# Performance work log

Hardware: AMD Instinct MI355X
Metric: run time of the kernel (lower is better)

Reference implementation:

```python
import jax, jax.numpy as jnp
import numpy as np

B, N, D_U = 32, 4096, 64
D = 128          # mlp_dim == model dim after MLP
H = 2            # n_heads
DH = D // H


def setup_inputs() -> dict:
    key = jax.random.key(0)
    ks = jax.random.split(key, 16)
    sc = lambda fan_in: 1.0 / np.sqrt(fan_in)
    inp = {
        "u": jax.random.normal(ks[0], (B, N, D_U), dtype=jnp.float32),
        "x": jax.random.uniform(ks[1], (B, N, 2), dtype=jnp.float32),
        # MLP params: [D_U -> D -> D], gelu after each hidden layer
        "W1": jax.random.normal(ks[2], (D_U, D), dtype=jnp.float32) * sc(D_U),
        "b1": jnp.zeros((D,), jnp.float32),
        "W2": jax.random.normal(ks[3], (D, D), dtype=jnp.float32) * sc(D),
        "b2": jnp.zeros((D,), jnp.float32),
        # learned pooling query (nn.Embed(1, D))
        "embed": jax.random.normal(ks[4], (1, D), dtype=jnp.float32),
        # multihead linear attention projections
        "Wq": jax.random.normal(ks[5], (D, D), dtype=jnp.float32) * sc(D),
        "bq": jnp.zeros((D,), jnp.float32),
        "Wk": jax.random.normal(ks[6], (D, D), dtype=jnp.float32) * sc(D),
        "bk": jnp.zeros((D,), jnp.float32),
        "Wv": jax.random.normal(ks[7], (D, D), dtype=jnp.float32) * sc(D),
        "bv": jnp.zeros((D,), jnp.float32),
        "Wo": jax.random.normal(ks[8], (D, D), dtype=jnp.float32) * sc(D),
        "bo": jnp.zeros((D,), jnp.float32),
    }
    return inp


def reference(u, x, W1, b1, W2, b2, embed, Wq, bq, Wk, bk, Wv, bv, Wo, bo):
    # MLP on set elements: [B, N, D_U] -> [B, N, D]
    z = jax.nn.gelu(u @ W1 + b1)
    z = jax.nn.gelu(z @ W2 + b2)

    n = z.shape[1]
    # learned query broadcast over batch: [B, 1, D]
    s = jnp.broadcast_to(embed[None, :, :], (z.shape[0], 1, z.shape[-1]))

    # multihead linear (Galerkin-style, softmax-free) attention
    q = (s @ Wq + bq).reshape(z.shape[0], 1, H, DH)   # [B, 1, H, DH]
    k = (z @ Wk + bk).reshape(z.shape[0], n, H, DH)   # [B, N, H, DH]
    v = (z @ Wv + bv).reshape(z.shape[0], n, H, DH)   # [B, N, H, DH]

    # context = K^T V / N per head: [B, H, DH, DH]
    context = jnp.einsum("bnhd,bnhe->bhde", k, v) / n
    out = jnp.einsum("bqhd,bhde->bqhe", q, context)   # [B, 1, H, DH]
    out = out.reshape(z.shape[0], 1, D) @ Wo + bo     # [B, 1, D]

    return out[:, 0, :]                               # [B, D]
```

## Files before the change

### kernel.cpp

```cpp
#include <hip/hip_runtime.h>
#include <math.h>

#define Bsz 32
#define Nn  4096
#define DU  64
#define Dm  128

#define GRID_MLP 256
#define BPB 8

#define WS_WKQ 0
#define WS_BKQ 256
#define WS_CNT 288
#define WS_A   320
#define WS_S   384
#define WS_WP  8576

#define H1STR 136

typedef short frag_ab __attribute__((ext_vector_type(8)));
typedef float frag_cd __attribute__((ext_vector_type(4)));

__device__ __forceinline__ unsigned short f2bf(float x) {
    union { float f; unsigned int u; } c; c.f = x;
    unsigned int r = c.u + 0x7fffu + ((c.u >> 16) & 1u);
    return (unsigned short)(r >> 16);
}

__device__ __forceinline__ float gelu_fast(float x) {
    float t = x * x;
    float a = x * fmaf(t, -0.1029432f, -2.3022081f);
    float e = __builtin_amdgcn_exp2f(a);
    return x * __builtin_amdgcn_rcpf(1.0f + e);
}

__global__ __launch_bounds__(256) void precompute_kernel(
    const float* __restrict__ embed, const float* __restrict__ Wq,
    const float* __restrict__ bq, const float* __restrict__ Wk,
    const float* __restrict__ bk, const float* __restrict__ W1,
    const float* __restrict__ W2, float* __restrict__ ws)
{
    __shared__ float qv[128];
    const int tid = threadIdx.x;
    const int bid = blockIdx.x;

    if (bid < 12) {
        const int e = bid * 256 + tid;
        const int f = e >> 6, L = e & 63;
        const int quad = L >> 4, n = L & 15;
        const float* src;
        int ks, nt;
        if (f < 16) { src = W1; ks = f >> 3;        nt = f & 7; }
        else        { src = W2; ks = (f - 16) >> 3; nt = (f - 16) & 7; }
        const int kb = ks * 32 + quad * 8;
        const int c  = nt * 16 + n;
        unsigned int p[4];
        #pragma unroll
        for (int jj = 0; jj < 4; ++jj) {
            unsigned int lo = f2bf(src[(kb + 2 * jj)     * Dm + c]);
            unsigned int hi = f2bf(src[(kb + 2 * jj + 1) * Dm + c]);
            p[jj] = lo | (hi << 16);
        }
        ((uint4*)(ws + WS_WP))[e] = make_uint4(p[0], p[1], p[2], p[3]);
    } else {
        if (tid < 128) {
            float s = bq[tid];
            #pragma unroll 8
            for (int j = 0; j < 128; ++j) s += embed[j] * Wq[j * 128 + tid];
            qv[tid] = s;
        }
        __syncthreads();
        if (tid < 128) {
            float s0 = 0.f, s1 = 0.f;
            #pragma unroll 8
            for (int dh = 0; dh < 64; ++dh) {
                s0 += Wk[tid * 128 + dh]      * qv[dh];
                s1 += Wk[tid * 128 + 64 + dh] * qv[64 + dh];
            }
            ws[WS_WKQ + tid]       = s0;
            ws[WS_WKQ + 128 + tid] = s1;
        }
        if (tid < 2) {
            float s = 0.f;
            for (int dh = 0; dh < 64; ++dh) s += bk[tid * 64 + dh] * qv[tid * 64 + dh];
            ws[WS_BKQ + tid] = s;
        }
    }
}

__global__ __launch_bounds__(1024) void mlp_pool_kernel(
    const float* __restrict__ u,  const float* __restrict__ b1,
    const float* __restrict__ b2, const float* __restrict__ Wv,
    const float* __restrict__ bv, const float* __restrict__ Wo,
    const float* __restrict__ bo, float* __restrict__ ws,
    float* __restrict__ out)
{
    __shared__ short  lds_w[48 * 512];
    __shared__ short  lds_h1[8 * 16 * H1STR];
    __shared__ float2 a2buf[8 * 16 * 2];
    __shared__ int    do_epi;

    const int tid  = threadIdx.x;
    const int wave = tid >> 6;
    const int lane = tid & 63;
    const int quad = lane >> 4;
    const int n15  = lane & 15;
    const int p    = wave >> 1;
    const int hf   = wave & 1;

    {
        const float4* src = (const float4*)(ws + WS_WP);
        float4* dst = (float4*)lds_w;
        dst[tid]        = src[tid];
        dst[tid + 1024] = src[tid + 1024];
        dst[tid + 2048] = src[tid + 2048];
    }

    float b1c[4], b2c[4], wkq0[4], wkq1[4];
    #pragma unroll
    for (int nt = 0; nt < 4; ++nt) {
        const int c = hf * 64 + nt * 16 + n15;
        b1c[nt]  = b1[c];
        b2c[nt]  = b2[c];
        wkq0[nt] = ws[WS_WKQ + c];
        wkq1[nt] = ws[WS_WKQ + 128 + c];
    }
    const float bkq0 = ws[WS_BKQ];
    const float bkq1 = ws[WS_BKQ + 1];
    __syncthreads();

    const int bb = blockIdx.x >> 3;
    const int jb = blockIdx.x & 7;
    short* h1t = lds_h1 + p * 16 * H1STR;

    float s0p[4], s1p[4];
    #pragma unroll
    for (int nt = 0; nt < 4; ++nt) { s0p[nt] = 0.f; s1p[nt] = 0.f; }
    float aA0 = 0.f, aA1 = 0.f;

    #pragma unroll 1
    for (int it = 0; it < 4; ++it) {
        const float* up = u + ((size_t)(bb * Nn + jb * 512 + it * 128 + p * 16 + n15)) * DU + quad * 8;
        float4 f0 = *(const float4*)(up);
        float4 f1 = *(const float4*)(up + 4);
        float4 f2 = *(const float4*)(up + 32);
        float4 f3 = *(const float4*)(up + 36);

        frag_ab a0, a1;
        a0[0] = (short)f2bf(f0.x); a0[1] = (short)f2bf(f0.y);
        a0[2] = (short)f2bf(f0.z); a0[3] = (short)f2bf(f0.w);
        a0[4] = (short)f2bf(f1.x); a0[5] = (short)f2bf(f1.y);
        a0[6] = (short)f2bf(f1.z); a0[7] = (short)f2bf(f1.w);
        a1[0] = (short)f2bf(f2.x); a1[1] = (short)f2bf(f2.y);
        a1[2] = (short)f2bf(f2.z); a1[3] = (short)f2bf(f2.w);
        a1[4] = (short)f2bf(f3.x); a1[5] = (short)f2bf(f3.y);
        a1[6] = (short)f2bf(f3.z); a1[7] = (short)f2bf(f3.w);

        frag_cd acc[4];
        #pragma unroll
        for (int nt = 0; nt < 4; ++nt) acc[nt] = (frag_cd){0.f, 0.f, 0.f, 0.f};
        #pragma unroll
        for (int nt = 0; nt < 4; ++nt) {
            const int f = hf * 4 + nt;
            frag_ab w0 = *(const frag_ab*)&lds_w[(f)     * 512 + lane * 8];
            acc[nt] = __builtin_amdgcn_mfma_f32_16x16x32_bf16(a0, w0, acc[nt], 0, 0, 0);
            frag_ab w1 = *(const frag_ab*)&lds_w[(8 + f) * 512 + lane * 8];
            acc[nt] = __builtin_amdgcn_mfma_f32_16x16x32_bf16(a1, w1, acc[nt], 0, 0, 0);
        }

        #pragma unroll
        for (int nt = 0; nt < 4; ++nt) {
            #pragma unroll
            for (int r = 0; r < 4; ++r) {
                float g = gelu_fast(acc[nt][r] + b1c[nt]);
                h1t[(quad * 4 + r) * H1STR + hf * 64 + nt * 16 + n15] = (short)f2bf(g);
            }
        }
        __syncthreads();

        frag_cd acc2[4];
        #pragma unroll
        for (int nt = 0; nt < 4; ++nt) acc2[nt] = (frag_cd){0.f, 0.f, 0.f, 0.f};
        #pragma unroll
        for (int ks = 0; ks < 4; ++ks) {
            frag_ab a2 = *(const frag_ab*)&h1t[n15 * H1STR + ks * 32 + quad * 8];
            #pragma unroll
            for (int nt = 0; nt < 4; ++nt) {
                frag_ab w2f = *(const frag_ab*)&lds_w[(16 + ks * 8 + hf * 4 + nt) * 512 + lane * 8];
                acc2[nt] = __builtin_amdgcn_mfma_f32_16x16x32_bf16(a2, w2f, acc2[nt], 0, 0, 0);
            }
        }

        #pragma unroll
        for (int nt = 0; nt < 4; ++nt) {
            #pragma unroll
            for (int r = 0; r < 4; ++r)
                acc2[nt][r] = gelu_fast(acc2[nt][r] + b2c[nt]);
        }

        float p0[4], p1[4];
        #pragma unroll
        for (int r = 0; r < 4; ++r) { p0[r] = 0.f; p1[r] = 0.f; }
        #pragma unroll
        for (int nt = 0; nt < 4; ++nt) {
            #pragma unroll
            for (int r = 0; r < 4; ++r) {
                p0[r] += acc2[nt][r] * wkq0[nt];
                p1[r] += acc2[nt][r] * wkq1[nt];
            }
        }
        #pragma unroll
        for (int r = 0; r < 4; ++r) {
            #pragma unroll
            for (int d = 1; d < 16; d <<= 1) {
                p0[r] += __shfl_xor(p0[r], d);
                p1[r] += __shfl_xor(p1[r], d);
            }
        }
        if (n15 == 0) {
            float* ab = (float*)a2buf;
            #pragma unroll
            for (int r = 0; r < 4; ++r) {
                const int row = quad * 4 + r;
                ab[(p * 32 + row * 2 + 0) * 2 + hf] = p0[r];
                ab[(p * 32 + row * 2 + 1) * 2 + hf] = p1[r];
            }
        }
        __syncthreads();

        #pragma unroll
        for (int r = 0; r < 4; ++r) {
            const int row = quad * 4 + r;
            float2 v0 = a2buf[p * 32 + row * 2 + 0];
            float2 v1 = a2buf[p * 32 + row * 2 + 1];
            const float al0 = v0.x + v0.y + bkq0;
            const float al1 = v1.x + v1.y + bkq1;
            #pragma unroll
            for (int nt = 0; nt < 4; ++nt) {
                s0p[nt] += al0 * acc2[nt][r];
                s1p[nt] += al1 * acc2[nt][r];
            }
            aA0 += al0; aA1 += al1;
        }
    }

    #pragma unroll
    for (int nt = 0; nt < 4; ++nt) {
        s0p[nt] += __shfl_xor(s0p[nt], 16); s0p[nt] += __shfl_xor(s0p[nt], 32);
        s1p[nt] += __shfl_xor(s1p[nt], 16); s1p[nt] += __shfl_xor(s1p[nt], 32);
    }
    aA0 += __shfl_xor(aA0, 16); aA0 += __shfl_xor(aA0, 32);
    aA1 += __shfl_xor(aA1, 16); aA1 += __shfl_xor(aA1, 32);

    if (quad == 0) {
        #pragma unroll
        for (int nt = 0; nt < 4; ++nt) {
            const int c = hf * 64 + nt * 16 + n15;
            atomicAdd(&ws[WS_S + (bb * 2 + 0) * 128 + c], s0p[nt]);
            atomicAdd(&ws[WS_S + (bb * 2 + 1) * 128 + c], s1p[nt]);
        }
    }
    if (hf == 0 && lane == 0) {
        atomicAdd(&ws[WS_A + bb * 2 + 0], aA0);
        atomicAdd(&ws[WS_A + bb * 2 + 1], aA1);
    }

    __syncthreads();
    if (tid == 0) {
        __threadfence();
        int old = atomicAdd((int*)ws + WS_CNT + bb, 1);
        do_epi = (old == BPB - 1) ? 1 : 0;
    }
    __syncthreads();

    if (do_epi) {
        float* eb     = (float*)lds_h1;
        float* e_sS   = eb;
        float* e_sA   = eb + 256;
        float* e_pool = eb + 264;
        float* e_part = eb + 392;

        if (tid < 256) e_sS[tid] = atomicAdd(&ws[WS_S + bb * 256 + tid], 0.f);
        if (tid < 2)   e_sA[tid] = atomicAdd(&ws[WS_A + bb * 2 + tid], 0.f);
        __syncthreads();

        const int i = tid & 127, seg = tid >> 7;
        const int h = i >> 6;
        if (tid < 512) {
            float dot = 0.f;
            #pragma unroll 8
            for (int d0 = 0; d0 < 32; ++d0) {
                const int d = seg * 32 + d0;
                dot += e_sS[h * 128 + d] * Wv[d * 128 + i];
            }
            e_part[tid] = dot;
        }
        __syncthreads();
        if (tid < 128)
            e_pool[i] = (e_part[i] + e_part[128 + i] + e_part[256 + i] + e_part[384 + i]
                         + e_sA[h] * bv[i]) * (1.0f / 4096.0f);
        __syncthreads();

        if (tid < 512) {
            float o = 0.f;
            #pragma unroll 8
            for (int d0 = 0; d0 < 32; ++d0) {
                const int d = seg * 32 + d0;
                o += e_pool[d] * Wo[d * 128 + i];
            }
            e_part[tid] = o;
        }
        __syncthreads();
        if (tid < 128)
            out[bb * 128 + i] = bo[i] + e_part[i] + e_part[128 + i] + e_part[256 + i] + e_part[384 + i];
    }
}

extern "C" void kernel_launch(void* const* d_in, const int* in_sizes, int n_in,
                              void* d_out, int out_size, void* d_ws, size_t ws_size,
                              hipStream_t stream) {
    const float* u     = (const float*)d_in[0];
    const float* W1    = (const float*)d_in[2];
    const float* b1    = (const float*)d_in[3];
    const float* W2    = (const float*)d_in[4];
    const float* b2    = (const float*)d_in[5];
    const float* embed = (const float*)d_in[6];
    const float* Wq    = (const float*)d_in[7];
    const float* bq    = (const float*)d_in[8];
    const float* Wk    = (const float*)d_in[9];
    const float* bk    = (const float*)d_in[10];
    const float* Wv    = (const float*)d_in[11];
    const float* bv    = (const float*)d_in[12];
    const float* Wo    = (const float*)d_in[13];
    const float* bo    = (const float*)d_in[14];
    float* ws  = (float*)d_ws;
    float* out = (float*)d_out;

    hipMemsetAsync((char*)d_ws + WS_CNT * 4, 0, (WS_WP - WS_CNT) * 4, stream);
    hipLaunchKernelGGL(precompute_kernel, dim3(13), dim3(256), 0, stream,
                       embed, Wq, bq, Wk, bk, W1, W2, ws);
    hipLaunchKernelGGL(mlp_pool_kernel, dim3(GRID_MLP), dim3(1024), 0, stream,
                       u, b1, b2, Wv, bv, Wo, bo, ws, out);
}
```

Baseline: 156.2 us.

## Fuse precompute into main kernel, prefetch u and double-buffer pooling stage

Removes the separate precompute kernel. Each block now packs W1/W2 into bf16 MFMA layout directly in LDS and computes Wk·q locally, which saves a launch and a global round trip. The main loop prefetches the next u tile into registers and double-buffers h1 and the alpha buffers. The alpha-weighted accumulation is deferred by one iteration so one __syncthreads per iteration can be dropped. In exchange, every one of the 256 blocks redundantly repacks the weights and computes the q projection. It also uses more LDS and registers.

```diff
diff --git a/kernel.cpp b/kernel.cpp
--- a/kernel.cpp
+++ b/kernel.cpp
@@ -9,12 +9,10 @@
 #define GRID_MLP 256
 #define BPB 8
 
-#define WS_WKQ 0
-#define WS_BKQ 256
 #define WS_CNT 288
 #define WS_A   320
 #define WS_S   384
-#define WS_WP  8576
+#define WS_END 8576
 
 #define H1STR 136
 
@@ -34,71 +32,21 @@
     return x * __builtin_amdgcn_rcpf(1.0f + e);
 }
 
-__global__ __launch_bounds__(256) void precompute_kernel(
-    const float* __restrict__ embed, const float* __restrict__ Wq,
-    const float* __restrict__ bq, const float* __restrict__ Wk,
-    const float* __restrict__ bk, const float* __restrict__ W1,
-    const float* __restrict__ W2, float* __restrict__ ws)
+__global__ __launch_bounds__(1024) void fused_mlp_pool_kernel(
+    const float* __restrict__ u,   const float* __restrict__ W1,
+    const float* __restrict__ b1,  const float* __restrict__ W2,
+    const float* __restrict__ b2,  const float* __restrict__ embed,
+    const float* __restrict__ Wq,  const float* __restrict__ bq,
+    const float* __restrict__ Wk,  const float* __restrict__ bk,
+    const float* __restrict__ Wv,  const float* __restrict__ bv,
+    const float* __restrict__ Wo,  const float* __restrict__ bo,
+    float* __restrict__ ws, float* __restrict__ out)
 {
-    __shared__ float qv[128];
-    const int tid = threadIdx.x;
-    const int bid = blockIdx.x;
-
-    if (bid < 12) {
-        const int e = bid * 256 + tid;
-        const int f = e >> 6, L = e & 63;
-        const int quad = L >> 4, n = L & 15;
-        const float* src;
-        int ks, nt;
-        if (f < 16) { src = W1; ks = f >> 3;        nt = f & 7; }
-        else        { src = W2; ks = (f - 16) >> 3; nt = (f - 16) & 7; }
-        const int kb = ks * 32 + quad * 8;
-        const int c  = nt * 16 + n;
-        unsigned int p[4];
-        #pragma unroll
-        for (int jj = 0; jj < 4; ++jj) {
-            unsigned int lo = f2bf(src[(kb + 2 * jj)     * Dm + c]);
-            unsigned int hi = f2bf(src[(kb + 2 * jj + 1) * Dm + c]);
-            p[jj] = lo | (hi << 16);
-        }
-        ((uint4*)(ws + WS_WP))[e] = make_uint4(p[0], p[1], p[2], p[3]);
-    } else {
-        if (tid < 128) {
-            float s = bq[tid];
-            #pragma unroll 8
-            for (int j = 0; j < 128; ++j) s += embed[j] * Wq[j * 128 + tid];
-            qv[tid] = s;
-        }
-        __syncthreads();
-        if (tid < 128) {
-            float s0 = 0.f, s1 = 0.f;
-            #pragma unroll 8
-            for (int dh = 0; dh < 64; ++dh) {
-                s0 += Wk[tid * 128 + dh]      * qv[dh];
-                s1 += Wk[tid * 128 + 64 + dh] * qv[64 + dh];
-            }
-            ws[WS_WKQ + tid]       = s0;
-            ws[WS_WKQ + 128 + tid] = s1;
-        }
-        if (tid < 2) {
-            float s = 0.f;
-            for (int dh = 0; dh < 64; ++dh) s += bk[tid * 64 + dh] * qv[tid * 64 + dh];
-            ws[WS_BKQ + tid] = s;
-        }
-    }
-}
-
-__global__ __launch_bounds__(1024) void mlp_pool_kernel(
-    const float* __restrict__ u,  const float* __restrict__ b1,
-    const float* __restrict__ b2, const float* __restrict__ Wv,
-    const float* __restrict__ bv, const float* __restrict__ Wo,
-    const float* __restrict__ bo, float* __restrict__ ws,
-    float* __restrict__ out)
-{
-    __shared__ short  lds_w[48 * 512];
-    __shared__ short  lds_h1[8 * 16 * H1STR];
-    __shared__ float2 a2buf[8 * 16 * 2];
-    __shared__ int    do_epi;
+    __shared__ short lds_w[48 * 512];
+    __shared__ short lds_h1[2][8 * 16 * H1STR];
+    __shared__ float a2buf[2][8][16][2][2];
+    __shared__ float lds_c[258];
+    __shared__ int   do_epi;
 
     const int tid  = threadIdx.x;
     const int wave = tid >> 6;
@@ -108,13 +56,49 @@
     const int p    = wave >> 1;
     const int hf   = wave & 1;
 
-    {
-        const float4* src = (const float4*)(ws + WS_WP);
-        float4* dst = (float4*)lds_w;
-        dst[tid]        = src[tid];
-        dst[tid + 1024] = src[tid + 1024];
-        dst[tid + 2048] = src[tid + 2048];
-    }
+    float* qtmp = (float*)a2buf;
+    if (tid < 128) {
+        float s = bq[tid];
+        #pragma unroll 8
+        for (int j = 0; j < 128; ++j) s += embed[j] * Wq[j * 128 + tid];
+        qtmp[tid] = s;
+    } else {
+        for (int e = tid - 128; e < 3072; e += 896) {
+            const int f = e >> 6, L = e & 63;
+            const int q2 = L >> 4, n = L & 15;
+            const float* src;
+            int ks, nt;
+            if (f < 16) { src = W1; ks = f >> 3;        nt = f & 7; }
+            else        { src = W2; ks = (f - 16) >> 3; nt = (f - 16) & 7; }
+            const int kb = ks * 32 + q2 * 8;
+            const int c  = nt * 16 + n;
+            unsigned int pk[4];
+            #pragma unroll
+            for (int jj = 0; jj < 4; ++jj) {
+                unsigned int lo = f2bf(src[(kb + 2 * jj)     * Dm + c]);
+                unsigned int hi = f2bf(src[(kb + 2 * jj + 1) * Dm + c]);
+                pk[jj] = lo | (hi << 16);
+            }
+            ((uint4*)lds_w)[e] = make_uint4(pk[0], pk[1], pk[2], pk[3]);
+        }
+    }
+    __syncthreads();
+    if (tid < 128) {
+        float s0 = 0.f, s1 = 0.f;
+        #pragma unroll 8
+        for (int dh = 0; dh < 64; ++dh) {
+            s0 += Wk[tid * 128 + dh]      * qtmp[dh];
+            s1 += Wk[tid * 128 + 64 + dh] * qtmp[64 + dh];
+        }
+        lds_c[tid]       = s0;
+        lds_c[128 + tid] = s1;
+    }
+    if (tid < 2) {
+        float s = 0.f;
+        for (int dh = 0; dh < 64; ++dh) s += bk[tid * 64 + dh] * qtmp[tid * 64 + dh];
+        lds_c[256 + tid] = s;
+    }
+    __syncthreads();
 
     float b1c[4], b2c[4], wkq0[4], wkq1[4];
     #pragma unroll
@@ -122,30 +106,30 @@
         const int c = hf * 64 + nt * 16 + n15;
         b1c[nt]  = b1[c];
         b2c[nt]  = b2[c];
-        wkq0[nt] = ws[WS_WKQ + c];
-        wkq1[nt] = ws[WS_WKQ + 128 + c];
-    }
-    const float bkq0 = ws[WS_BKQ];
-    const float bkq1 = ws[WS_BKQ + 1];
-    __syncthreads();
+        wkq0[nt] = lds_c[c];
+        wkq1[nt] = lds_c[128 + c];
+    }
+    const float bkq0 = lds_c[256];
+    const float bkq1 = lds_c[257];
 
     const int bb = blockIdx.x >> 3;
     const int jb = blockIdx.x & 7;
-    short* h1t = lds_h1 + p * 16 * H1STR;
 
     float s0p[4], s1p[4];
     #pragma unroll
     for (int nt = 0; nt < 4; ++nt) { s0p[nt] = 0.f; s1p[nt] = 0.f; }
     float aA0 = 0.f, aA1 = 0.f;
+    frag_cd zprev[4];
+    int cur = 0;
+
+    const float* ub = u + ((size_t)(bb * Nn + jb * 512 + p * 16 + n15)) * DU + quad * 8;
+    float4 f0 = *(const float4*)(ub);
+    float4 f1 = *(const float4*)(ub + 4);
+    float4 f2 = *(const float4*)(ub + 32);
+    float4 f3 = *(const float4*)(ub + 36);
 
     #pragma unroll 1
     for (int it = 0; it < 4; ++it) {
-        const float* up = u + ((size_t)(bb * Nn + jb * 512 + it * 128 + p * 16 + n15)) * DU + quad * 8;
-        float4 f0 = *(const float4*)(up);
-        float4 f1 = *(const float4*)(up + 4);
-        float4 f2 = *(const float4*)(up + 32);
-        float4 f3 = *(const float4*)(up + 36);
-
         frag_ab a0, a1;
         a0[0] = (short)f2bf(f0.x); a0[1] = (short)f2bf(f0.y);
         a0[2] = (short)f2bf(f0.z); a0[3] = (short)f2bf(f0.w);
@@ -156,6 +140,14 @@
         a1[4] = (short)f2bf(f3.x); a1[5] = (short)f2bf(f3.y);
         a1[6] = (short)f2bf(f3.z); a1[7] = (short)f2bf(f3.w);
 
+        if (it < 3) {
+            const float* un = ub + (size_t)((it + 1) * 128) * DU;
+            f0 = *(const float4*)(un);
+            f1 = *(const float4*)(un + 4);
+            f2 = *(const float4*)(un + 32);
+            f3 = *(const float4*)(un + 36);
+        }
+
         frag_cd acc[4];
         #pragma unroll
         for (int nt = 0; nt < 4; ++nt) acc[nt] = (frag_cd){0.f, 0.f, 0.f, 0.f};
@@ -168,6 +160,7 @@
             acc[nt] = __builtin_amdgcn_mfma_f32_16x16x32_bf16(a1, w1, acc[nt], 0, 0, 0);
         }
 
+        short* h1t = lds_h1[cur] + p * 16 * H1STR;
         #pragma unroll
         for (int nt = 0; nt < 4; ++nt) {
             #pragma unroll
@@ -178,6 +171,22 @@
         }
         __syncthreads();
 
+        if (it > 0) {
+            const int pb = 1 - cur;
+            #pragma unroll
+            for (int r = 0; r < 4; ++r) {
+                const int row = quad * 4 + r;
+                const float al0 = a2buf[pb][p][row][0][0] + a2buf[pb][p][row][0][1] + bkq0;
+                const float al1 = a2buf[pb][p][row][1][0] + a2buf[pb][p][row][1][1] + bkq1;
+                #pragma unroll
+                for (int nt = 0; nt < 4; ++nt) {
+                    s0p[nt] += al0 * zprev[nt][r];
+                    s1p[nt] += al1 * zprev[nt][r];
+                }
+                aA0 += al0; aA1 += al1;
+            }
+        }
+
         frag_cd acc2[4];
         #pragma unroll
         for (int nt = 0; nt < 4; ++nt) acc2[nt] = (frag_cd){0.f, 0.f, 0.f, 0.f};
@@ -218,27 +227,30 @@
             }
         }
         if (n15 == 0) {
-            float* ab = (float*)a2buf;
             #pragma unroll
             for (int r = 0; r < 4; ++r) {
                 const int row = quad * 4 + r;
-                ab[(p * 32 + row * 2 + 0) * 2 + hf] = p0[r];
-                ab[(p * 32 + row * 2 + 1) * 2 + hf] = p1[r];
-            }
-        }
-        __syncthreads();
-
+                a2buf[cur][p][row][0][hf] = p0[r];
+                a2buf[cur][p][row][1][hf] = p1[r];
+            }
+        }
+        #pragma unroll
+        for (int nt = 0; nt < 4; ++nt) zprev[nt] = acc2[nt];
+        cur ^= 1;
+    }
+
+    __syncthreads();
+    {
+        const int pb = 1 - cur;
         #pragma unroll
         for (int r = 0; r < 4; ++r) {
             const int row = quad * 4 + r;
-            float2 v0 = a2buf[p * 32 + row * 2 + 0];
-            float2 v1 = a2buf[p * 32 + row * 2 + 1];
-            const float al0 = v0.x + v0.y + bkq0;
-            const float al1 = v1.x + v1.y + bkq1;
+            const float al0 = a2buf[pb][p][row][0][0] + a2buf[pb][p][row][0][1] + bkq0;
+            const float al1 = a2buf[pb][p][row][1][0] + a2buf[pb][p][row][1][1] + bkq1;
             #pragma unroll
             for (int nt = 0; nt < 4; ++nt) {
-                s0p[nt] += al0 * acc2[nt][r];
-                s1p[nt] += al1 * acc2[nt][r];
+                s0p[nt] += al0 * zprev[nt][r];
+                s1p[nt] += al1 * zprev[nt][r];
             }
             aA0 += al0; aA1 += al1;
         }
@@ -336,9 +348,7 @@
     float* ws  = (float*)d_ws;
     float* out = (float*)d_out;
 
-    hipMemsetAsync((char*)d_ws + WS_CNT * 4, 0, (WS_WP - WS_CNT) * 4, stream);
-    hipLaunchKernelGGL(precompute_kernel, dim3(13), dim3(256), 0, stream,
-                       embed, Wq, bq, Wk, bk, W1, W2, ws);
-    hipLaunchKernelGGL(mlp_pool_kernel, dim3(GRID_MLP), dim3(1024), 0, stream,
-                       u, b1, b2, Wv, bv, Wo, bo, ws, out);
+    hipMemsetAsync((char*)d_ws + WS_CNT * 4, 0, (WS_END - WS_CNT) * 4, stream);
+    hipLaunchKernelGGL(fused_mlp_pool_kernel, dim3(GRID_MLP), dim3(1024), 0, stream,
+                       u, W1, b1, W2, b2, embed, Wq, bq, Wk, bk, Wv, bv, Wo, bo, ws, out);
 }
```

Result: no change. 155.5 us (-0.4%).

## Use smaller blocks over more of the grid, read packed weights from global, prefetch inputs

Applied to the files above, without the earlier changes.

Blocks shrink from 1024 to 512 threads and the grid grows from 256 to 1024 blocks, with 32 blocks per batch element each handling 128 rows in two iterations. The per-block LDS staging of the packed bf16 weights and its barrier are removed, so MFMA weight fragments are now read directly from global memory, relying on L2/L1 caching. The next iteration's u rows are software-prefetched into registers. The aim is more occupancy and less per-block setup, at the cost of repeated global weight reads and more atomic contention on the per-batch counters and accumulators.

```diff
diff --git a/kernel.cpp b/kernel.cpp
--- a/kernel.cpp
+++ b/kernel.cpp
@@ -6,8 +6,8 @@
 #define DU  64
 #define Dm  128
 
-#define GRID_MLP 256
-#define BPB 8
+#define GRID_MLP 1024
+#define BPB 32
 
 #define WS_WKQ 0
 #define WS_BKQ 256
@@ -47,12 +47,12 @@
     if (bid < 12) {
         const int e = bid * 256 + tid;
         const int f = e >> 6, L = e & 63;
-        const int quad = L >> 4, n = L & 15;
+        const int q2 = L >> 4, n = L & 15;
         const float* src;
         int ks, nt;
         if (f < 16) { src = W1; ks = f >> 3;        nt = f & 7; }
         else        { src = W2; ks = (f - 16) >> 3; nt = (f - 16) & 7; }
-        const int kb = ks * 32 + quad * 8;
+        const int kb = ks * 32 + q2 * 8;
         const int c  = nt * 16 + n;
         unsigned int p[4];
         #pragma unroll
@@ -88,17 +88,16 @@
     }
 }
 
-__global__ __launch_bounds__(1024) void mlp_pool_kernel(
+__global__ __launch_bounds__(512) void mlp_pool_kernel(
     const float* __restrict__ u,  const float* __restrict__ b1,
     const float* __restrict__ b2, const float* __restrict__ Wv,
     const float* __restrict__ bv, const float* __restrict__ Wo,
     const float* __restrict__ bo, float* __restrict__ ws,
     float* __restrict__ out)
 {
-    __shared__ short  lds_w[48 * 512];
-    __shared__ short  lds_h1[8 * 16 * H1STR];
-    __shared__ float2 a2buf[8 * 16 * 2];
-    __shared__ int    do_epi;
+    __shared__ short lds_h1[4 * 16 * H1STR];
+    __shared__ float a2buf[4][16][2][2];
+    __shared__ int   do_epi;
 
     const int tid  = threadIdx.x;
     const int wave = tid >> 6;
@@ -108,13 +107,7 @@
     const int p    = wave >> 1;
     const int hf   = wave & 1;
 
-    {
-        const float4* src = (const float4*)(ws + WS_WP);
-        float4* dst = (float4*)lds_w;
-        dst[tid]        = src[tid];
-        dst[tid + 1024] = src[tid + 1024];
-        dst[tid + 2048] = src[tid + 2048];
-    }
+    const short* wst = (const short*)(ws + WS_WP) + lane * 8;
 
     float b1c[4], b2c[4], wkq0[4], wkq1[4];
     #pragma unroll
@@ -127,10 +120,9 @@
     }
     const float bkq0 = ws[WS_BKQ];
     const float bkq1 = ws[WS_BKQ + 1];
-    __syncthreads();
-
-    const int bb = blockIdx.x >> 3;
-    const int jb = blockIdx.x & 7;
+
+    const int bb = blockIdx.x >> 5;
+    const int jb = blockIdx.x & 31;
     short* h1t = lds_h1 + p * 16 * H1STR;
 
     float s0p[4], s1p[4];
@@ -138,14 +130,14 @@
     for (int nt = 0; nt < 4; ++nt) { s0p[nt] = 0.f; s1p[nt] = 0.f; }
     float aA0 = 0.f, aA1 = 0.f;
 
+    const float* ub = u + ((size_t)(bb * Nn + jb * 128 + p * 16 + n15)) * DU + quad * 8;
+    float4 f0 = *(const float4*)(ub);
+    float4 f1 = *(const float4*)(ub + 4);
+    float4 f2 = *(const float4*)(ub + 32);
+    float4 f3 = *(const float4*)(ub + 36);
+
     #pragma unroll 1
-    for (int it = 0; it < 4; ++it) {
-        const float* up = u + ((size_t)(bb * Nn + jb * 512 + it * 128 + p * 16 + n15)) * DU + quad * 8;
-        float4 f0 = *(const float4*)(up);
-        float4 f1 = *(const float4*)(up + 4);
-        float4 f2 = *(const float4*)(up + 32);
-        float4 f3 = *(const float4*)(up + 36);
-
+    for (int it = 0; it < 2; ++it) {
         frag_ab a0, a1;
         a0[0] = (short)f2bf(f0.x); a0[1] = (short)f2bf(f0.y);
         a0[2] = (short)f2bf(f0.z); a0[3] = (short)f2bf(f0.w);
@@ -156,15 +148,23 @@
         a1[4] = (short)f2bf(f3.x); a1[5] = (short)f2bf(f3.y);
         a1[6] = (short)f2bf(f3.z); a1[7] = (short)f2bf(f3.w);
 
+        if (it < 1) {
+            const float* un = ub + (size_t)(64 * DU);
+            f0 = *(const float4*)(un);
+            f1 = *(const float4*)(un + 4);
+            f2 = *(const float4*)(un + 32);
+            f3 = *(const float4*)(un + 36);
+        }
+
         frag_cd acc[4];
         #pragma unroll
         for (int nt = 0; nt < 4; ++nt) acc[nt] = (frag_cd){0.f, 0.f, 0.f, 0.f};
         #pragma unroll
         for (int nt = 0; nt < 4; ++nt) {
             const int f = hf * 4 + nt;
-            frag_ab w0 = *(const frag_ab*)&lds_w[(f)     * 512 + lane * 8];
+            frag_ab w0 = *(const frag_ab*)(wst + (f)     * 512);
             acc[nt] = __builtin_amdgcn_mfma_f32_16x16x32_bf16(a0, w0, acc[nt], 0, 0, 0);
-            frag_ab w1 = *(const frag_ab*)&lds_w[(8 + f) * 512 + lane * 8];
+            frag_ab w1 = *(const frag_ab*)(wst + (8 + f) * 512);
             acc[nt] = __builtin_amdgcn_mfma_f32_16x16x32_bf16(a1, w1, acc[nt], 0, 0, 0);
         }
 
@@ -186,7 +186,7 @@
             frag_ab a2 = *(const frag_ab*)&h1t[n15 * H1STR + ks * 32 + quad * 8];
             #pragma unroll
             for (int nt = 0; nt < 4; ++nt) {
-                frag_ab w2f = *(const frag_ab*)&lds_w[(16 + ks * 8 + hf * 4 + nt) * 512 + lane * 8];
+                frag_ab w2f = *(const frag_ab*)(wst + (16 + ks * 8 + hf * 4 + nt) * 512);
                 acc2[nt] = __builtin_amdgcn_mfma_f32_16x16x32_bf16(a2, w2f, acc2[nt], 0, 0, 0);
             }
         }
@@ -218,12 +218,11 @@
             }
         }
         if (n15 == 0) {
-            float* ab = (float*)a2buf;
             #pragma unroll
             for (int r = 0; r < 4; ++r) {
                 const int row = quad * 4 + r;
-                ab[(p * 32 + row * 2 + 0) * 2 + hf] = p0[r];
-                ab[(p * 32 + row * 2 + 1) * 2 + hf] = p1[r];
+                a2buf[p][row][0][hf] = p0[r];
+                a2buf[p][row][1][hf] = p1[r];
             }
         }
         __syncthreads();
@@ -231,10 +230,8 @@
         #pragma unroll
         for (int r = 0; r < 4; ++r) {
             const int row = quad * 4 + r;
-            float2 v0 = a2buf[p * 32 + row * 2 + 0];
-            float2 v1 = a2buf[p * 32 + row * 2 + 1];
-            const float al0 = v0.x + v0.y + bkq0;
-            const float al1 = v1.x + v1.y + bkq1;
+            const float al0 = a2buf[p][row][0][0] + a2buf[p][row][0][1] + bkq0;
+            const float al1 = a2buf[p][row][1][0] + a2buf[p][row][1][1] + bkq1;
             #pragma unroll
             for (int nt = 0; nt < 4; ++nt) {
                 s0p[nt] += al0 * acc2[nt][r];
@@ -286,7 +283,7 @@
 
         const int i = tid & 127, seg = tid >> 7;
         const int h = i >> 6;
-        if (tid < 512) {
+        {
             float dot = 0.f;
             #pragma unroll 8
             for (int d0 = 0; d0 < 32; ++d0) {
@@ -301,7 +298,7 @@
                          + e_sA[h] * bv[i]) * (1.0f / 4096.0f);
         __syncthreads();
 
-        if (tid < 512) {
+        {
             float o = 0.f;
             #pragma unroll 8
             for (int d0 = 0; d0 < 32; ++d0) {
@@ -339,6 +336,6 @@
     hipMemsetAsync((char*)d_ws + WS_CNT * 4, 0, (WS_WP - WS_CNT) * 4, stream);
     hipLaunchKernelGGL(precompute_kernel, dim3(13), dim3(256), 0, stream,
                        embed, Wq, bq, Wk, bk, W1, W2, ws);
-    hipLaunchKernelGGL(mlp_pool_kernel, dim3(GRID_MLP), dim3(1024), 0, stream,
+    hipLaunchKernelGGL(mlp_pool_kernel, dim3(GRID_MLP), dim3(512), 0, stream,
                        u, b1, b2, Wv, bv, Wo, bo, ws, out);
 }
```

Measured after the change: 207.2 us. +32.7%, slower.
